# Performance work log

Hardware: AMD Instinct MI355X
Metric: run time of the kernel (lower is better)

Reference implementation:

```python
import jax, jax.numpy as jnp
import numpy as np

B, S, H, D = 4, 4096, 8, 128
EPS = 1e-6


def layernorm(x, g, b, axes):
    m = jnp.mean(x, axis=axes, keepdims=True)
    v = jnp.mean(jnp.square(x - m), axis=axes, keepdims=True)
    return (x - m) / jnp.sqrt(v + EPS) * g + b


def setup_inputs() -> dict:
    key = jax.random.key(0)
    ks = jax.random.split(key, 6)
    scale = 0.05
    return {
        "heads_input": jax.random.normal(ks[0], (B, S, H, D), jnp.float32),
        # GroupLinear trans_hid: per-head (2D -> 3D)
        "W_hid": jax.random.normal(ks[1], (H, 2 * D, 3 * D), jnp.float32) * scale,
        "b_hid": jax.random.normal(ks[2], (H, 3 * D), jnp.float32) * scale,
        # GroupLinear trans_og: per-head (2D -> D)
        "W_og": jax.random.normal(ks[3], (H, 2 * D, D), jnp.float32) * scale,
        "b_og": jax.random.normal(ks[4], (H, D), jnp.float32) * scale,
        # LayerNorm affine params (elementwise_affine=True)
        "ln_csum_g": jnp.ones((H, D), jnp.float32),
        "ln_csum_b": jnp.zeros((H, D), jnp.float32),
        "ln_hid_g": jnp.ones((H, 3, D), jnp.float32),
        "ln_hid_b": jnp.zeros((H, 3, D), jnp.float32),
        "ln_og_g": jnp.ones((H, D), jnp.float32),
        "ln_og_b": jnp.zeros((H, D), jnp.float32),
        "init_cx": jnp.zeros((1, H, D), jnp.float32),
    }


def reference(heads_input, W_hid, b_hid, W_og, b_og, ln_csum_g, ln_csum_b,
              ln_hid_g, ln_hid_b, ln_og_g, ln_og_b, init_cx):
    b, s, h, d = heads_input.shape
    # shifted cumulative sum over time, then LayerNorm over (head, dim)
    shifted = jnp.concatenate(
        [jnp.zeros((b, 1, h, d), heads_input.dtype), heads_input[:, :-1]], axis=1)
    csum = layernorm(jnp.cumsum(shifted, axis=1), ln_csum_g, ln_csum_b, (-2, -1))
    cat = jnp.concatenate([heads_input, csum], axis=-1)        # [b,s,h,2d]
    hid = jnp.einsum('bshi,hio->bsho', cat, W_hid) + b_hid     # [b,s,h,3d]
    hid = layernorm(hid.reshape(b, s, h, 3, d), ln_hid_g, ln_hid_b, (-3, -2, -1))
    igate, fgate, hidden = hid[..., 0, :], hid[..., 1, :], hid[..., 2, :]
    fgate = jax.nn.sigmoid(fgate)
    igh = jax.nn.sigmoid(igate) * jax.nn.relu(hidden)
    # LGateFunc: cell_t = fgate_t * cell_{t-1} + igh_t, cell_0 = init_cx
    c0 = jnp.broadcast_to(init_cx, (b, h, d)).astype(heads_input.dtype)
    def step(c, fi):
        f, i = fi
        c = f * c + i
        return c, c
    _, cells = jax.lax.scan(step, c0,
                            (fgate.transpose(1, 0, 2, 3), igh.transpose(1, 0, 2, 3)))
    cell = cells.transpose(1, 0, 2, 3)                          # [b,s,h,d]
    og_in = jnp.concatenate([heads_input, cell], axis=-1)       # [b,s,h,2d]
    og = layernorm(jnp.einsum('bshi,hio->bsho', og_in, W_og) + b_og,
                   ln_og_g, ln_og_b, (-2, -1))
    return jax.nn.sigmoid(og) * cell
```

## Files before the change

### kernel.cpp

```cpp
#include <hip/hip_runtime.h>

#define EPSF 1e-6f


typedef __attribute__((ext_vector_type(8))) short short8v;
typedef __attribute__((ext_vector_type(4))) float float4v;

__device__ __forceinline__ float sigm(float x) { return 1.0f / (1.0f + __expf(-x)); }

__device__ __forceinline__ unsigned short f2bf(float f) {
    unsigned int u = __float_as_uint(f);
    u = (u + 0x7fffu + ((u >> 16) & 1u)) >> 16;
    return (unsigned short)u;
}
__device__ __forceinline__ float bf2f(unsigned short s) { return __uint_as_float(((unsigned int)s) << 16); }
__device__ __forceinline__ float bf2f_lo(unsigned int p) { return __uint_as_float(p << 16); }
__device__ __forceinline__ float bf2f_hi(unsigned int p) { return __uint_as_float(p & 0xffff0000u); }
__device__ __forceinline__ unsigned int pack2bf(float a, float b) {
    return (unsigned int)f2bf(a) | ((unsigned int)f2bf(b) << 16);
}

__device__ __forceinline__ void block_reduce2(float& a, float& b) {
#pragma unroll
    for (int off = 32; off > 0; off >>= 1) {
        a += __shfl_down(a, off);
        b += __shfl_down(b, off);
    }
    __shared__ float sa[8], sb[8];
    int wid = threadIdx.x >> 6;
    int lane = threadIdx.x & 63;
    if (lane == 0) { sa[wid] = a; sb[wid] = b; }
    __syncthreads();
    a = sa[0] + sa[1] + sa[2] + sa[3];
    b = sb[0] + sb[1] + sb[2] + sb[3];
}

__global__ __launch_bounds__(256) void k_prep_w(const float* __restrict__ Wh, const float* __restrict__ Wo,
                                                unsigned short* __restrict__ WTH,
                                                unsigned short* __restrict__ WTO) {
    int idx = blockIdx.x * 256 + threadIdx.x;
    if (idx < 786432) {
        int k = idx & 255;
        int rest = idx >> 8;
        int o = rest % 384;
        int h = rest / 384;
        WTH[idx] = f2bf(Wh[((size_t)h * 256 + k) * 384 + o]);
    } else {
        int i2 = idx - 786432;
        int k = i2 & 255;
        int rest = i2 >> 8;
        int o = rest & 127;
        int h = rest >> 7;
        WTO[i2] = f2bf(Wo[((size_t)h * 256 + k) * 128 + o]);
    }
}

__global__ __launch_bounds__(256) void k_cumsum_a(const float* __restrict__ X, float* __restrict__ cS,
                                                  unsigned short* __restrict__ XB) {
    int t = blockIdx.x * 256 + threadIdx.x;
    int d = t & 127, h = (t >> 7) & 7, k = (t >> 10) & 63, b = t >> 16;
    size_t xbase = (((size_t)(b * 4096 + k * 64)) * 8 + h) * 128 + d;
    size_t pbase = ((size_t)h * 16384 + b * 4096 + k * 64) * 128 + d;
    float s = 0.f;
    for (int j = 0; j < 64; ++j) {
        unsigned short xb = f2bf(X[xbase + (size_t)j * 1024]);
        XB[pbase + (size_t)j * 128] = xb;
        s += bf2f(xb);
    }
    cS[(size_t)((b * 8 + h) * 128 + d) * 64 + k] = s;
}

__global__ __launch_bounds__(256) void k_cumsum_b(const float* __restrict__ cS, float* __restrict__ cO) {
    int wave = (blockIdx.x * 256 + threadIdx.x) >> 6;
    int lane = threadIdx.x & 63;
    size_t idx = (size_t)wave * 64 + lane;
    float v = cS[idx];
    float incl = v;
#pragma unroll
    for (int d = 1; d < 64; d <<= 1) {
        float t = __shfl_up(incl, d);
        if (lane >= d) incl += t;
    }
    cO[idx] = incl - v;
}

__global__ __launch_bounds__(256) void k_cumsum_c(const unsigned short* __restrict__ XB,
                                                  const float* __restrict__ cO,
                                                  unsigned short* __restrict__ CSUMB) {
    int t = blockIdx.x * 256 + threadIdx.x;
    int d = t & 127, h = (t >> 7) & 7, k = (t >> 10) & 63, b = t >> 16;
    int ch = (b * 8 + h) * 128 + d;
    float run = cO[(size_t)ch * 64 + k];
    size_t pbase = ((size_t)h * 16384 + b * 4096 + k * 64) * 128 + d;
    for (int j = 0; j < 64; ++j) {
        float x = bf2f(XB[pbase + (size_t)j * 128]);
        CSUMB[pbase + (size_t)j * 128] = f2bf(run);
        run += x;
    }
}

__global__ __launch_bounds__(256) void k_ln_csum(const unsigned short* __restrict__ CSUMB,
                                                 unsigned short* __restrict__ CSB,
                                                 const float* __restrict__ g, const float* __restrict__ bb) {
    int bs = blockIdx.x, t = threadIdx.x;
    int h = t >> 5, c = t & 31;
    size_t u2i = ((size_t)h * 16384 + bs) * 32 + c;
    uint2 u = ((const uint2*)CSUMB)[u2i];
    float4 v;
    v.x = bf2f_lo(u.x); v.y = bf2f_hi(u.x);
    v.z = bf2f_lo(u.y); v.w = bf2f_hi(u.y);
    float s = v.x + v.y + v.z + v.w;
    float ss = v.x * v.x + v.y * v.y + v.z * v.z + v.w * v.w;
    block_reduce2(s, ss);
    float m = s * (1.f / 1024.f);
    float var = ss * (1.f / 1024.f) - m * m;
    float r = rsqrtf(fmaxf(var, 0.f) + EPSF);
    float4 gv = ((const float4*)g)[t];
    float4 bv = ((const float4*)bb)[t];
    uint2 o;
    o.x = pack2bf((v.x - m) * r * gv.x + bv.x, (v.y - m) * r * gv.y + bv.y);
    o.y = pack2bf((v.z - m) * r * gv.z + bv.z, (v.w - m) * r * gv.w + bv.w);
    ((uint2*)CSB)[u2i] = o;
}

__global__ __launch_bounds__(512) void k_gemm_bf16(const unsigned short* __restrict__ A1,
                                                   const unsigned short* __restrict__ A2,
                                                   const unsigned short* __restrict__ Wt,
                                                   const float* __restrict__ bias,
                                                   unsigned short* __restrict__ OUT, int Nw, int m0,
                                                   int nbx) {
    __shared__ short As[4][8192];
    __shared__ short Bs[4][8192];
    int bid = blockIdx.x;
    int h = bid & 7;
    int rest = bid >> 3;
    int bx = rest % nbx;
    int by = rest / nbx;
    int t0 = threadIdx.x;
    int lane = t0 & 63, wid = t0 >> 6;
    int wr = wid >> 1, wc = wid & 1;
    int l15 = lane & 15, l4 = lane >> 4;
    int lr = lane >> 3, lc = lane & 7;
    const int bxc = bx * 128;
    const size_t mbase = (size_t)(m0 + by * 128);
    const size_t aplane = (size_t)h * 16384;

    float4v acc[2][4];
#pragma unroll
    for (int i = 0; i < 2; ++i)
#pragma unroll
        for (int j = 0; j < 4; ++j) acc[i][j] = (float4v)(0.f);

    auto STAGE = [&](int t) {
        const unsigned short* src = (t < 2) ? A1 : A2;
        int kofs = (t & 1) * 64;
#pragma unroll
        for (int it = 0; it < 2; ++it) {
            int r0 = wid * 16 + it * 8;
            int r = r0 + lr;
            int c = lc ^ (r & 7);
            size_t g = (aplane + mbase + r) * 128 + kofs + c * 8;
            __builtin_amdgcn_global_load_lds((const __attribute__((address_space(1))) void*)(src + g),
                                             (__attribute__((address_space(3))) void*)(&As[t][r0 * 64]),
                                             16, 0, 0);
        }
#pragma unroll
        for (int it = 0; it < 2; ++it) {
            int n0 = wid * 16 + it * 8;
            int cl = n0 + lr;
            int c = lc ^ (cl & 7);
            size_t g = ((size_t)(h * Nw + bxc + cl)) * 256 + t * 64 + c * 8;
            __builtin_amdgcn_global_load_lds((const __attribute__((address_space(1))) void*)(Wt + g),
                                             (__attribute__((address_space(3))) void*)(&Bs[t][n0 * 64]),
                                             16, 0, 0);
        }
    };

    STAGE(0); STAGE(1); STAGE(2); STAGE(3);

#pragma unroll
    for (int t = 0; t < 4; ++t) {
        if (t == 0)      asm volatile("s_waitcnt vmcnt(12)" ::: "memory");
        else if (t == 1) asm volatile("s_waitcnt vmcnt(8)" ::: "memory");
        else if (t == 2) asm volatile("s_waitcnt vmcnt(4)" ::: "memory");
        else             asm volatile("s_waitcnt vmcnt(0)" ::: "memory");
        __builtin_amdgcn_s_barrier();
        __builtin_amdgcn_sched_barrier(0);
#pragma unroll
        for (int kk = 0; kk < 2; ++kk) {
            short8v a[2], b[4];
#pragma unroll
            for (int i = 0; i < 2; ++i) {
                int r = wr * 32 + i * 16 + l15;
                int slot = (kk * 4 + l4) ^ (r & 7);
                a[i] = *(const short8v*)(&As[t][r * 64 + slot * 8]);
            }
#pragma unroll
            for (int j = 0; j < 4; ++j) {
                int c = wc * 64 + j * 16 + l15;
                int slot = (kk * 4 + l4) ^ (c & 7);
                b[j] = *(const short8v*)(&Bs[t][c * 64 + slot * 8]);
            }
#pragma unroll
            for (int i = 0; i < 2; ++i)
#pragma unroll
                for (int j = 0; j < 4; ++j)
                    acc[i][j] = __builtin_amdgcn_mfma_f32_16x16x32_bf16(a[i], b[j], acc[i][j], 0, 0, 0);
        }
    }

    __syncthreads();
    short* Cs = &As[0][0];
#pragma unroll
    for (int j = 0; j < 4; ++j) {
        int col = wc * 64 + j * 16 + l15;
        float bv = bias[h * Nw + bxc + col];
#pragma unroll
        for (int i = 0; i < 2; ++i) {
            int rbase = wr * 32 + i * 16 + l4 * 4;
#pragma unroll
            for (int q = 0; q < 4; ++q) {
                Cs[(rbase + q) * 136 + col] = f2bf(acc[i][j][q] + bv);
            }
        }
    }
    __syncthreads();
    {
        int row = t0 >> 2, seg = t0 & 3;
        const uint4* src = (const uint4*)(Cs + row * 136 + seg * 32);
        size_t gb = ((size_t)(by * 128 + row) * 8 + h) * Nw + bxc + seg * 32;
        uint4 v0 = src[0], v1 = src[1], v2 = src[2], v3 = src[3];
        *(uint4*)(&OUT[gb]) = v0;
        *(uint4*)(&OUT[gb + 8]) = v1;
        *(uint4*)(&OUT[gb + 16]) = v2;
        *(uint4*)(&OUT[gb + 24]) = v3;
    }
}

__global__ __launch_bounds__(256) void k_ln_gates(const unsigned short* __restrict__ HID,
                                                  unsigned short* __restrict__ FG,
                                                  unsigned short* __restrict__ IG,
                                                  const float* __restrict__ g, const float* __restrict__ bb,
                                                  int m0) {
    __shared__ float sm[3072];
    int bsl = blockIdx.x, t = threadIdx.x;
    int bs = m0 + bsl;
    const uint4* row = (const uint4*)(HID + (size_t)bsl * 3072);
    float s = 0.f, ss = 0.f;
    for (int idx = t; idx < 384; idx += 256) {
        uint4 u = row[idx];
        float f0 = bf2f_lo(u.x), f1 = bf2f_hi(u.x);
        float f2 = bf2f_lo(u.y), f3 = bf2f_hi(u.y);
        float f4 = bf2f_lo(u.z), f5 = bf2f_hi(u.z);
        float f6 = bf2f_lo(u.w), f7 = bf2f_hi(u.w);
        float* p = sm + idx * 8;
        p[0] = f0; p[1] = f1; p[2] = f2; p[3] = f3; p[4] = f4; p[5] = f5; p[6] = f6; p[7] = f7;
        s += f0 + f1 + f2 + f3 + f4 + f5 + f6 + f7;
        ss += f0 * f0 + f1 * f1 + f2 * f2 + f3 * f3 + f4 * f4 + f5 * f5 + f6 * f6 + f7 * f7;
    }
    block_reduce2(s, ss);
    float m = s * (1.f / 3072.f);
    float var = ss * (1.f / 3072.f) - m * m;
    float r = rsqrtf(fmaxf(var, 0.f) + EPSF);
    int u0 = t * 4;
    int h = u0 >> 7;
    int d0 = u0 & 127;
    float fr[4], ir[4];
#pragma unroll
    for (int q = 0; q < 4; ++q) {
        int d = d0 + q;
        float yi = sm[h * 384 + d];
        float yf = sm[h * 384 + 128 + d];
        float yh = sm[h * 384 + 256 + d];
        float ni = (yi - m) * r * g[(h * 3 + 0) * 128 + d] + bb[(h * 3 + 0) * 128 + d];
        float nf = (yf - m) * r * g[(h * 3 + 1) * 128 + d] + bb[(h * 3 + 1) * 128 + d];
        float nh = (yh - m) * r * g[(h * 3 + 2) * 128 + d] + bb[(h * 3 + 2) * 128 + d];
        fr[q] = sigm(nf);
        ir[q] = sigm(ni) * fmaxf(nh, 0.f);
    }
    uint2 fo, io;
    fo.x = pack2bf(fr[0], fr[1]); fo.y = pack2bf(fr[2], fr[3]);
    io.x = pack2bf(ir[0], ir[1]); io.y = pack2bf(ir[2], ir[3]);
    ((uint2*)(FG + (size_t)bs * 1024))[t] = fo;
    ((uint2*)(IG + (size_t)bs * 1024))[t] = io;
}

__global__ __launch_bounds__(256) void k_scan_a(const unsigned short* __restrict__ FG,
                                                const unsigned short* __restrict__ IG,
                                                float* __restrict__ cF, float* __restrict__ cC) {
    int t = blockIdx.x * 256 + threadIdx.x;
    int d2 = t & 63, h = (t >> 6) & 7, k = (t >> 9) & 63, b = t >> 15;
    size_t base = (((size_t)(b * 4096 + k * 64)) * 8 + h) * 64 + d2;
    const unsigned int* FGu = (const unsigned int*)FG;
    const unsigned int* IGu = (const unsigned int*)IG;
    float F0 = 1.f, C0 = 0.f, F1 = 1.f, C1 = 0.f;
    for (int j = 0; j < 64; ++j) {
        unsigned int fg = FGu[base + (size_t)j * 512];
        unsigned int ig = IGu[base + (size_t)j * 512];
        float f0 = bf2f_lo(fg), f1 = bf2f_hi(fg);
        C0 = fmaf(f0, C0, bf2f_lo(ig)); F0 *= f0;
        C1 = fmaf(f1, C1, bf2f_hi(ig)); F1 *= f1;
    }
    size_t ci0 = ((size_t)((b * 8 + h) * 128 + d2 * 2)) * 64 + k;
    cF[ci0] = F0; cC[ci0] = C0;
    cF[ci0 + 64] = F1; cC[ci0 + 64] = C1;
}

__global__ __launch_bounds__(256) void k_scan_b(const float* __restrict__ cF, const float* __restrict__ cC,
                                                const float* __restrict__ initcx, float* __restrict__ cI) {
    int wave = (blockIdx.x * 256 + threadIdx.x) >> 6;
    int lane = threadIdx.x & 63;
    size_t idx = (size_t)wave * 64 + lane;
    float F = cF[idx], C = cC[idx];
#pragma unroll
    for (int d = 1; d < 64; d <<= 1) {
        float Fp = __shfl_up(F, d);
        float Cp = __shfl_up(C, d);
        if (lane >= d) { C = fmaf(Cp, F, C); F *= Fp; }
    }
    float Fe = __shfl_up(F, 1);
    float Ce = __shfl_up(C, 1);
    if (lane == 0) { Fe = 1.f; Ce = 0.f; }
    float c0 = initcx[wave & 1023];
    cI[idx] = fmaf(Fe, c0, Ce);
}

__global__ __launch_bounds__(256) void k_scan_c(const unsigned short* __restrict__ FG,
                                                const unsigned short* __restrict__ IG,
                                                unsigned short* __restrict__ CLB,
                                                const float* __restrict__ cI) {
    int t = blockIdx.x * 256 + threadIdx.x;
    int d2 = t & 63, h = (t >> 6) & 7, k = (t >> 9) & 63, b = t >> 15;
    size_t base = (((size_t)(b * 4096 + k * 64)) * 8 + h) * 64 + d2;
    size_t pbase = ((size_t)h * 16384 + b * 4096 + k * 64) * 64 + d2;
    const unsigned int* FGu = (const unsigned int*)FG;
    const unsigned int* IGu = (const unsigned int*)IG;
    unsigned int* CLu = (unsigned int*)CLB;
    size_t ci0 = ((size_t)((b * 8 + h) * 128 + d2 * 2)) * 64 + k;
    float c0 = cI[ci0], c1 = cI[ci0 + 64];
    for (int j = 0; j < 64; ++j) {
        unsigned int fg = FGu[base + (size_t)j * 512];
        unsigned int ig = IGu[base + (size_t)j * 512];
        c0 = fmaf(bf2f_lo(fg), c0, bf2f_lo(ig));
        c1 = fmaf(bf2f_hi(fg), c1, bf2f_hi(ig));
        CLu[pbase + (size_t)j * 64] = pack2bf(c0, c1);
    }
}

__global__ __launch_bounds__(256) void k_ln_out(const unsigned short* __restrict__ OG,
                                                const unsigned short* __restrict__ CLB,
                                                const float* __restrict__ g, const float* __restrict__ bb,
                                                float* __restrict__ OUT, int m0) {
    int bsl = blockIdx.x, t = threadIdx.x;
    int bs = m0 + bsl;
    uint2 u = ((const uint2*)(OG + (size_t)bsl * 1024))[t];
    float4 v;
    v.x = bf2f_lo(u.x); v.y = bf2f_hi(u.x);
    v.z = bf2f_lo(u.y); v.w = bf2f_hi(u.y);
    float s = v.x + v.y + v.z + v.w;
    float ss = v.x * v.x + v.y * v.y + v.z * v.z + v.w * v.w;
    block_reduce2(s, ss);
    float m = s * (1.f / 1024.f);
    float var = ss * (1.f / 1024.f) - m * m;
    float r = rsqrtf(fmaxf(var, 0.f) + EPSF);
    float4 gv = ((const float4*)g)[t];
    float4 bv = ((const float4*)bb)[t];
    int h = t >> 5, c = t & 31;
    uint2 cu = ((const uint2*)CLB)[((size_t)h * 16384 + bs) * 32 + c];
    float4 cv;
    cv.x = bf2f_lo(cu.x); cv.y = bf2f_hi(cu.x);
    cv.z = bf2f_lo(cu.y); cv.w = bf2f_hi(cu.y);
    float4 o;
    o.x = sigm((v.x - m) * r * gv.x + bv.x) * cv.x;
    o.y = sigm((v.y - m) * r * gv.y + bv.y) * cv.y;
    o.z = sigm((v.z - m) * r * gv.z + bv.z) * cv.z;
    o.w = sigm((v.w - m) * r * gv.w + bv.w) * cv.w;
    ((float4*)(OUT + (size_t)bs * 1024))[t] = o;
}

extern "C" void kernel_launch(void* const* d_in, const int* in_sizes, int n_in,
                              void* d_out, int out_size, void* d_ws, size_t ws_size,
                              hipStream_t stream) {
    const float* X      = (const float*)d_in[0];
    const float* W_hid  = (const float*)d_in[1];
    const float* b_hid  = (const float*)d_in[2];
    const float* W_og   = (const float*)d_in[3];
    const float* b_og   = (const float*)d_in[4];
    const float* g_cs   = (const float*)d_in[5];
    const float* b_cs   = (const float*)d_in[6];
    const float* g_hid  = (const float*)d_in[7];
    const float* b_hidl = (const float*)d_in[8];
    const float* g_og   = (const float*)d_in[9];
    const float* b_ogl  = (const float*)d_in[10];
    const float* initcx = (const float*)d_in[11];

    float* ws = (float*)d_ws;
    const size_t O_SC    = 0ull;
    const size_t O_XB    = 1310720ull;
    const size_t O_CSUMB = 9699328ull;
    const size_t O_CSB   = 18087936ull;
    const size_t O_IGB   = 26476544ull;
    const size_t O_CLB   = 34865152ull;
    const size_t O_WTH   = 43253760ull;
    const size_t O_WTO   = 43646976ull;
    const size_t O_HID   = 43778048ull;

    float* cS = ws + O_SC;
    float* cO = cS + 262144;
    float* cF = cO + 262144;
    float* cC = cF + 262144;
    float* cI = cC + 262144;
    unsigned short* XB    = (unsigned short*)(ws + O_XB);
    unsigned short* CSUMB = (unsigned short*)(ws + O_CSUMB);
    unsigned short* FGB   = CSUMB;
    unsigned short* CSB   = (unsigned short*)(ws + O_CSB);
    unsigned short* IGB   = (unsigned short*)(ws + O_IGB);
    unsigned short* CLB   = (unsigned short*)(ws + O_CLB);
    unsigned short* WTH   = (unsigned short*)(ws + O_WTH);
    unsigned short* WTO   = (unsigned short*)(ws + O_WTO);
    unsigned short* HIDC  = (unsigned short*)(ws + O_HID);

    size_t avail = (ws_size / 4 > O_HID) ? ws_size / 4 - O_HID : 0;
    int CH = 1024;
    for (int c = 16384; c >= 1024; c >>= 1) {
        if ((size_t)c * 1536ull <= avail) { CH = c; break; }
    }
    const int NC = 16384 / CH;

    dim3 blk(256);
    dim3 blkg(512);
    k_prep_w<<<4096, blk, 0, stream>>>(W_hid, W_og, WTH, WTO);
    k_cumsum_a<<<1024, blk, 0, stream>>>(X, cS, XB);
    k_cumsum_b<<<1024, blk, 0, stream>>>(cS, cO);
    k_cumsum_c<<<1024, blk, 0, stream>>>(XB, cO, CSUMB);
    k_ln_csum<<<16384, blk, 0, stream>>>(CSUMB, CSB, g_cs, b_cs);
    for (int c = 0; c < NC; ++c) {
        int m0 = c * CH;
        k_gemm_bf16<<<8 * 3 * (CH / 128), blkg, 0, stream>>>(XB, CSB, WTH, b_hid, HIDC, 384, m0, 3);
        k_ln_gates<<<CH, blk, 0, stream>>>(HIDC, FGB, IGB, g_hid, b_hidl, m0);
    }
    k_scan_a<<<512, blk, 0, stream>>>(FGB, IGB, cF, cC);
    k_scan_b<<<1024, blk, 0, stream>>>(cF, cC, initcx, cI);
    k_scan_c<<<512, blk, 0, stream>>>(FGB, IGB, CLB, cI);
    for (int c = 0; c < NC; ++c) {
        int m0 = c * CH;
        k_gemm_bf16<<<8 * 1 * (CH / 128), blkg, 0, stream>>>(XB, CLB, WTO, b_og, HIDC, 128, m0, 1);
        k_ln_out<<<CH, blk, 0, stream>>>(HIDC, CLB, g_og, b_ogl, (float*)d_out, m0);
    }
}
```

Baseline: 279.4 us.

## Double-buffer GEMM K-stages and write output directly without LDS staging

The grouped GEMM kernel moves from four LDS stage buffers all loaded up front to two ping-pong buffers that prefetch the next K-stage while the current one is computed. This halves the kernel's shared memory, which may allow more resident blocks per CU. The epilogue drops the LDS transpose and writes bf16 results straight to global memory with scalar 2-byte stores. That removes two syncthreads but gives up coalesced 16-byte stores and adds a barrier per K-step.

After: 237.6 us (median of 2 runs). -15.0%, faster.

```diff
diff --git a/kernel.cpp b/kernel.cpp
--- a/kernel.cpp
+++ b/kernel.cpp
@@ -129,8 +129,8 @@
                                                    const float* __restrict__ bias,
                                                    unsigned short* __restrict__ OUT, int Nw, int m0,
                                                    int nbx) {
-    __shared__ short As[4][8192];
-    __shared__ short Bs[4][8192];
+    __shared__ short As[2][8192];
+    __shared__ short Bs[2][8192];
     int bid = blockIdx.x;
     int h = bid & 7;
     int rest = bid >> 3;
@@ -151,7 +151,7 @@
 #pragma unroll
         for (int j = 0; j < 4; ++j) acc[i][j] = (float4v)(0.f);
 
-    auto STAGE = [&](int t) {
+    auto STAGE = [&](int t, int buf) {
         const unsigned short* src = (t < 2) ? A1 : A2;
         int kofs = (t & 1) * 64;
 #pragma unroll
@@ -161,7 +161,7 @@
             int c = lc ^ (r & 7);
             size_t g = (aplane + mbase + r) * 128 + kofs + c * 8;
             __builtin_amdgcn_global_load_lds((const __attribute__((address_space(1))) void*)(src + g),
-                                             (__attribute__((address_space(3))) void*)(&As[t][r0 * 64]),
+                                             (__attribute__((address_space(3))) void*)(&As[buf][r0 * 64]),
                                              16, 0, 0);
         }
 #pragma unroll
@@ -171,19 +171,21 @@
             int c = lc ^ (cl & 7);
             size_t g = ((size_t)(h * Nw + bxc + cl)) * 256 + t * 64 + c * 8;
             __builtin_amdgcn_global_load_lds((const __attribute__((address_space(1))) void*)(Wt + g),
-                                             (__attribute__((address_space(3))) void*)(&Bs[t][n0 * 64]),
+                                             (__attribute__((address_space(3))) void*)(&Bs[buf][n0 * 64]),
                                              16, 0, 0);
         }
     };
 
-    STAGE(0); STAGE(1); STAGE(2); STAGE(3);
-
+    STAGE(0, 0);
 #pragma unroll
     for (int t = 0; t < 4; ++t) {
-        if (t == 0)      asm volatile("s_waitcnt vmcnt(12)" ::: "memory");
-        else if (t == 1) asm volatile("s_waitcnt vmcnt(8)" ::: "memory");
-        else if (t == 2) asm volatile("s_waitcnt vmcnt(4)" ::: "memory");
-        else             asm volatile("s_waitcnt vmcnt(0)" ::: "memory");
+        int cur = t & 1;
+        if (t < 3) {
+            STAGE(t + 1, cur ^ 1);
+            asm volatile("s_waitcnt vmcnt(4)" ::: "memory");
+        } else {
+            asm volatile("s_waitcnt vmcnt(0)" ::: "memory");
+        }
         __builtin_amdgcn_s_barrier();
         __builtin_amdgcn_sched_barrier(0);
 #pragma unroll
@@ -193,13 +195,13 @@
             for (int i = 0; i < 2; ++i) {
                 int r = wr * 32 + i * 16 + l15;
                 int slot = (kk * 4 + l4) ^ (r & 7);
-                a[i] = *(const short8v*)(&As[t][r * 64 + slot * 8]);
+                a[i] = *(const short8v*)(&As[cur][r * 64 + slot * 8]);
             }
 #pragma unroll
             for (int j = 0; j < 4; ++j) {
                 int c = wc * 64 + j * 16 + l15;
                 int slot = (kk * 4 + l4) ^ (c & 7);
-                b[j] = *(const short8v*)(&Bs[t][c * 64 + slot * 8]);
+                b[j] = *(const short8v*)(&Bs[cur][c * 64 + slot * 8]);
             }
 #pragma unroll
             for (int i = 0; i < 2; ++i)
@@ -207,33 +209,21 @@
                 for (int j = 0; j < 4; ++j)
                     acc[i][j] = __builtin_amdgcn_mfma_f32_16x16x32_bf16(a[i], b[j], acc[i][j], 0, 0, 0);
         }
-    }
-
-    __syncthreads();
-    short* Cs = &As[0][0];
+        __builtin_amdgcn_sched_barrier(0);
+        __builtin_amdgcn_s_barrier();
+    }
 #pragma unroll
     for (int j = 0; j < 4; ++j) {
-        int col = wc * 64 + j * 16 + l15;
-        float bv = bias[h * Nw + bxc + col];
+        int o = bxc + wc * 64 + j * 16 + l15;
+        float bv = bias[h * Nw + o];
 #pragma unroll
         for (int i = 0; i < 2; ++i) {
-            int rbase = wr * 32 + i * 16 + l4 * 4;
+            int mlb = by * 128 + wr * 32 + i * 16 + l4 * 4;
 #pragma unroll
             for (int q = 0; q < 4; ++q) {
-                Cs[(rbase + q) * 136 + col] = f2bf(acc[i][j][q] + bv);
+                OUT[((size_t)(mlb + q) * 8 + h) * Nw + o] = f2bf(acc[i][j][q] + bv);
             }
         }
-    }
-    __syncthreads();
-    {
-        int row = t0 >> 2, seg = t0 & 3;
-        const uint4* src = (const uint4*)(Cs + row * 136 + seg * 32);
-        size_t gb = ((size_t)(by * 128 + row) * 8 + h) * Nw + bxc + seg * 32;
-        uint4 v0 = src[0], v1 = src[1], v2 = src[2], v3 = src[3];
-        *(uint4*)(&OUT[gb]) = v0;
-        *(uint4*)(&OUT[gb + 8]) = v1;
-        *(uint4*)(&OUT[gb + 16]) = v2;
-        *(uint4*)(&OUT[gb + 24]) = v3;
     }
 }
 
```
